# Performance work log

Hardware: AMD Instinct MI355X
Metric: run time of the kernel (lower is better)

## Reference

```python
import jax, jax.numpy as jnp
import numpy as np

TOKEN_SIZE = 16
STRIDE = 8
EMBED_DIM = 512


def setup_inputs() -> dict:
    key = jax.random.key(0)
    k1, k2 = jax.random.split(key)
    B, S, D = 32, 4096, EMBED_DIM
    x = jax.random.normal(k1, (B, S, D), dtype=jnp.float32)
    fan_in = TOKEN_SIZE * D
    W = jax.random.normal(k2, (fan_in, D), dtype=jnp.float32) / np.sqrt(fan_in)
    b = jnp.zeros((D,), dtype=jnp.float32)
    gamma = jnp.ones((D,), dtype=jnp.float32)
    beta = jnp.zeros((D,), dtype=jnp.float32)
    return {"x": x, "W": W, "b": b, "gamma": gamma, "beta": beta}


def reference(x, W, b, gamma, beta):
    B, S, D = x.shape
    n_win = (S - TOKEN_SIZE) // STRIDE + 1
    # gather all sliding windows at once: [n_win, token_size] index matrix
    idx = jnp.arange(n_win)[:, None] * STRIDE + jnp.arange(TOKEN_SIZE)[None, :]
    win = x[:, idx, :]                       # [B, n_win, token_size, D]
    win = win.reshape(B, n_win, TOKEN_SIZE * D)  # flatten each window
    h = jnp.einsum('bnf,fd->bnd', win, W) + b    # batched GEMM
    h = jax.nn.gelu(h, approximate=False)        # torch GELU default = exact erf
    # LayerNorm over last dim (eps matches torch default 1e-5)
    mu = jnp.mean(h, axis=-1, keepdims=True)
    var = jnp.var(h, axis=-1, keepdims=True)
    h = (h - mu) * jax.lax.rsqrt(var + 1e-5)
    return h * gamma + beta                      # [B, n_win, D]
```

## Files before the change

### kernel.cpp

```cpp
#include <hip/hip_runtime.h>
#include <hip/hip_bf16.h>
#include <cstdint>

#define S_LEN 4096
#define D_DIM 512
#define NWIN  511
#define KDIM  8192
#define THREADS 512

typedef __attribute__((ext_vector_type(8))) short short8;
typedef __attribute__((ext_vector_type(4))) float f32x4;

__device__ __forceinline__ unsigned short f2b(float f) {
    union { float f; unsigned int u; } v; v.f = f;
    unsigned int r = v.u + 0x7FFFu + ((v.u >> 16) & 1u);
    return (unsigned short)(r >> 16);
}

__global__ void wpack_kernel(const float* __restrict__ W, short8* __restrict__ pk) {
    __shared__ float tile[64][68];
    const int b2 = blockIdx.x;
    const int s = b2 >> 3, w = b2 & 7;
    const int t = s >> 3, c0 = (s & 7) << 6;
    const int tid = threadIdx.x;
    {
        int r = tid >> 2, c4 = (tid & 3) << 4;
        const float* src = W + (size_t)(t * 512 + c0 + r) * D_DIM + (w << 6) + c4;
#pragma unroll
        for (int j = 0; j < 4; ++j) {
            float4 v = *(const float4*)(src + 4 * j);
            tile[r][c4 + 4 * j + 0] = v.x;
            tile[r][c4 + 4 * j + 1] = v.y;
            tile[r][c4 + 4 * j + 2] = v.z;
            tile[r][c4 + 4 * j + 3] = v.w;
        }
    }
    __syncthreads();
    const int lane = tid & 63, f2 = tid >> 6;
#pragma unroll
    for (int ff = 0; ff < 2; ++ff) {
        int f = f2 * 2 + ff;
        int n = f >> 1, k32 = f & 1;
        short8 u;
#pragma unroll
        for (int e = 0; e < 8; ++e)
            u[e] = (short)f2b(tile[k32 * 32 + (lane >> 4) * 8 + e][n * 16 + (lane & 15)]);
        pk[((size_t)b2 * 8 + f) * 64 + lane] = u;
    }
}

__device__ __forceinline__ void load_b(const short8* __restrict__ pk, int s, int wid,
                                       int lane, short8 (&b)[4][2]) {
    const short8* base = pk + ((size_t)(s * 8 + wid) * 8) * 64 + lane;
#pragma unroll
    for (int n = 0; n < 4; ++n)
#pragma unroll
        for (int k32 = 0; k32 < 2; ++k32)
            b[n][k32] = base[(n * 2 + k32) * 64];
}

__global__ __launch_bounds__(THREADS, 2)
void fused_kernel(const float* __restrict__ x,
                  const short8* __restrict__ pk,
                  const float* __restrict__ bias,
                  const float* __restrict__ gamma,
                  const float* __restrict__ beta,
                  float* __restrict__ out)
{
    __shared__ __align__(16) unsigned short lsA[2][64 * 64];
    __shared__ float redS[8][64];
    __shared__ float redQ[8][64];

    const int blk = blockIdx.x;
    const int b  = blk >> 3;
    const int n0 = (blk & 7) << 6;
    const int tid = threadIdx.x;
    const int lane = tid & 63;
    const int wid  = tid >> 6;
    const int r15 = lane & 15, hi = lane >> 4;
    const int ai = tid >> 3, ak8 = tid & 7;
    const int akb = ak8 ^ (ai & 7);
    const float* xb = x + (size_t)b * S_LEN * D_DIM;

    f32x4 acc[4][4] = {};
    short8 bc[4][2], bn[4][2];

    {
        int row = 8 * (n0 + ai) + 0;
        if (row > S_LEN - 1) row = S_LEN - 1;
        const float* src = xb + (size_t)row * D_DIM + 0 + ak8 * 8;
        float4 f0 = *(const float4*)src;
        float4 f1 = *(const float4*)(src + 4);
        short8 u;
        u[0] = (short)f2b(f0.x); u[1] = (short)f2b(f0.y);
        u[2] = (short)f2b(f0.z); u[3] = (short)f2b(f0.w);
        u[4] = (short)f2b(f1.x); u[5] = (short)f2b(f1.y);
        u[6] = (short)f2b(f1.z); u[7] = (short)f2b(f1.w);
        *(short8*)&lsA[0][ai * 64 + akb * 8] = u;
        load_b(pk, 0, wid, lane, bc);
    }
    __syncthreads();

#define STEP(S, CUR, NXT, BCUR, BNXT)                                          \
    {                                                                          \
        const int sn = ((S) + 1) & 127;                                        \
                                            \
        const int tn = sn >> 3, c0n = (sn & 7) << 6;                           \
        int rown = 8 * (n0 + ai) + tn;                                         \
        if (rown > S_LEN - 1) rown = S_LEN - 1;                                \
        const float* asrc = xb + (size_t)rown * D_DIM + c0n + ak8 * 8;         \
        float4 f0 = *(const float4*)asrc;                                      \
        float4 f1 = *(const float4*)(asrc + 4);                                \
                                   \
        load_b(pk, sn, wid, lane, BNXT);                                       \
                                               \
        short8 afr[4][2];                                                      \
        _Pragma("unroll")                                                      \
        for (int m = 0; m < 4; ++m) {                                          \
            int row = 16 * m + r15;                                            \
            _Pragma("unroll")                                                  \
            for (int k32 = 0; k32 < 2; ++k32) {                                \
                int kb = (k32 * 4 + hi) ^ (row & 7);                           \
                afr[m][k32] = *(const short8*)&lsA[CUR][row * 64 + kb * 8];    \
            }                                                                  \
        }                                                                      \
               \
        _Pragma("unroll")                                                      \
        for (int k32 = 0; k32 < 2; ++k32)                                      \
            _Pragma("unroll")                                                  \
            for (int m = 0; m < 4; ++m)                                        \
                _Pragma("unroll")                                              \
                for (int n = 0; n < 4; ++n)                                    \
                    acc[m][n] = __builtin_amdgcn_mfma_f32_16x16x32_bf16(       \
                        afr[m][k32], BCUR[n][k32], acc[m][n], 0, 0, 0);        \
           \
        short8 u;                                                              \
        u[0] = (short)f2b(f0.x); u[1] = (short)f2b(f0.y);                      \
        u[2] = (short)f2b(f0.z); u[3] = (short)f2b(f0.w);                      \
        u[4] = (short)f2b(f1.x); u[5] = (short)f2b(f1.y);                      \
        u[6] = (short)f2b(f1.z); u[7] = (short)f2b(f1.w);                      \
        *(short8*)&lsA[NXT][ai * 64 + akb * 8] = u;                            \
        asm volatile("s_waitcnt lgkmcnt(0)" ::: "memory");                     \
        __builtin_amdgcn_s_barrier();                                          \
        __builtin_amdgcn_sched_barrier(0);                                     \
    }

    for (int it = 0; it < 64; ++it) {
        STEP(it * 2,     0, 1, bc, bn)
        STEP(it * 2 + 1, 1, 0, bn, bc)
    }
#undef STEP

    float bias4[4], gam4[4], bet4[4];
#pragma unroll
    for (int n = 0; n < 4; ++n) {
        int d = (wid << 6) + 16 * n + r15;
        bias4[n] = bias[d]; gam4[n] = gamma[d]; bet4[n] = beta[d];
    }
    float sum_[4][4], sq_[4][4];
#pragma unroll
    for (int m = 0; m < 4; ++m)
#pragma unroll
        for (int r = 0; r < 4; ++r) { sum_[m][r] = 0.f; sq_[m][r] = 0.f; }
#pragma unroll
    for (int m = 0; m < 4; ++m)
#pragma unroll
        for (int n = 0; n < 4; ++n)
#pragma unroll
            for (int r = 0; r < 4; ++r) {
                float h = acc[m][n][r] + bias4[n];
                float g = 0.5f * h * (1.0f + erff(h * 0.70710678118654752f));
                acc[m][n][r] = g;
                sum_[m][r] += g;
                sq_[m][r]  += g * g;
            }
#pragma unroll
    for (int m = 0; m < 4; ++m)
#pragma unroll
        for (int r = 0; r < 4; ++r) {
            float sv = sum_[m][r], qv = sq_[m][r];
#pragma unroll
            for (int msk = 1; msk < 16; msk <<= 1) {
                sv += __shfl_xor(sv, msk, 64);
                qv += __shfl_xor(qv, msk, 64);
            }
            sum_[m][r] = sv; sq_[m][r] = qv;
        }
    if (r15 == 0) {
#pragma unroll
        for (int m = 0; m < 4; ++m)
#pragma unroll
            for (int r = 0; r < 4; ++r) {
                int row16 = 16 * m + hi * 4 + r;
                redS[wid][row16] = sum_[m][r];
                redQ[wid][row16] = sq_[m][r];
            }
    }
    __syncthreads();
#pragma unroll
    for (int m = 0; m < 4; ++m) {
#pragma unroll
        for (int r = 0; r < 4; ++r) {
            int row16 = 16 * m + hi * 4 + r;
            float sv = 0.f, qv = 0.f;
#pragma unroll
            for (int w = 0; w < 8; ++w) { sv += redS[w][row16]; qv += redQ[w][row16]; }
            float mu  = sv * (1.0f / 512.0f);
            float var = qv * (1.0f / 512.0f) - mu * mu;
            float inv = rsqrtf(var + 1e-5f);
            int win = n0 + row16;
            if (win < NWIN) {
                size_t obase = ((size_t)b * NWIN + win) * D_DIM;
#pragma unroll
                for (int n = 0; n < 4; ++n) {
                    int d = (wid << 6) + 16 * n + r15;
                    out[obase + d] = (acc[m][n][r] - mu) * inv * gam4[n] + bet4[n];
                }
            }
        }
    }
}

__global__ void naive_kernel(const float* __restrict__ x, const float* __restrict__ W,
                             const float* __restrict__ bias, const float* __restrict__ gamma,
                             const float* __restrict__ beta, float* __restrict__ out) {
    __shared__ float hrow[D_DIM];
    __shared__ float red[2];
    const int b = blockIdx.x / NWIN, win = blockIdx.x % NWIN;
    const int d = threadIdx.x;
    float a = 0.f;
    for (int t = 0; t < 16; ++t) {
        const float* xr = x + ((size_t)b * S_LEN + 8 * win + t) * D_DIM;
        const float* wr = W + (size_t)t * D_DIM * D_DIM;
        for (int k = 0; k < D_DIM; ++k) a += xr[k] * wr[(size_t)k * D_DIM + d];
    }
    a += bias[d];
    a = 0.5f * a * (1.0f + erff(a * 0.70710678118654752f));
    hrow[d] = a;
    __syncthreads();
    if (d == 0) {
        float s = 0.f, q = 0.f;
        for (int k = 0; k < D_DIM; ++k) { s += hrow[k]; q += hrow[k] * hrow[k]; }
        float mu = s / D_DIM;
        red[0] = mu; red[1] = rsqrtf(q / D_DIM - mu * mu + 1e-5f);
    }
    __syncthreads();
    out[((size_t)b * NWIN + win) * D_DIM + d] = (a - red[0]) * red[1] * gamma[d] + beta[d];
}

extern "C" void kernel_launch(void* const* d_in, const int* in_sizes, int n_in,
                              void* d_out, int out_size, void* d_ws, size_t ws_size,
                              hipStream_t stream) {
    const float* x     = (const float*)d_in[0];
    const float* W     = (const float*)d_in[1];
    const float* bias  = (const float*)d_in[2];
    const float* gamma = (const float*)d_in[3];
    const float* beta  = (const float*)d_in[4];
    float* out = (float*)d_out;

    const size_t pk_bytes = (size_t)KDIM * D_DIM * sizeof(unsigned short);
    if (ws_size >= pk_bytes) {
        short8* pk = (short8*)d_ws;
        wpack_kernel<<<1024, 256, 0, stream>>>(W, (short8*)pk);
        fused_kernel<<<256, THREADS, 0, stream>>>(x, pk, bias, gamma, beta, out);
    } else {
        naive_kernel<<<32 * NWIN, D_DIM, 0, stream>>>(x, W, bias, gamma, beta, out);
    }
}
```

Baseline: 196.0 us.

## Split fused kernel into reuse-staged GEMM+GELU and separate LayerNorm kernel

Replaces the single fused kernel with a GEMM kernel that stages a contiguous 520-row slab of x per column chunk into LDS, so the overlapping sliding windows share the loaded rows instead of each token offset being re-read from global memory. Each block now covers half the output columns with 256 threads, giving 512 blocks. The GELU output goes to a workspace buffer, and a separate wave-per-row LayerNorm kernel then normalises it. This cuts redundant x loads and bf16 conversions, at the cost of writing and re-reading an intermediate h tensor, one extra launch, and barriers between the staging phases. It also depends on a larger workspace being available.

```diff
diff --git a/kernel.cpp b/kernel.cpp
--- a/kernel.cpp
+++ b/kernel.cpp
@@ -6,7 +6,8 @@
 #define D_DIM 512
 #define NWIN  511
 #define KDIM  8192
-#define THREADS 512
+#define TROWS 520
+#define ASLOTS (TROWS * 8)
 
 typedef __attribute__((ext_vector_type(8))) short short8;
 typedef __attribute__((ext_vector_type(4))) float f32x4;
@@ -49,9 +50,9 @@
     }
 }
 
-__device__ __forceinline__ void load_b(const short8* __restrict__ pk, int s, int wid,
+__device__ __forceinline__ void load_b(const short8* __restrict__ pk, int s, int wslot,
                                        int lane, short8 (&b)[4][2]) {
-    const short8* base = pk + ((size_t)(s * 8 + wid) * 8) * 64 + lane;
+    const short8* base = pk + ((size_t)(s * 8 + wslot) * 8) * 64 + lane;
 #pragma unroll
     for (int n = 0; n < 4; ++n)
 #pragma unroll
@@ -59,7 +60,165 @@
             b[n][k32] = base[(n * 2 + k32) * 64];
 }
 
-__global__ __launch_bounds__(THREADS, 2)
+__device__ __forceinline__ void stage_a(const float* __restrict__ xb, int n0, int tid,
+                                        int c0, unsigned short* __restrict__ lsA) {
+#pragma unroll 4
+    for (int it = 0; it < 17; ++it) {
+        int slot = tid + (it << 8);
+        if (slot < ASLOTS) {
+            int r = slot >> 3, k8 = slot & 7;
+            int grow = 8 * n0 + r;
+            if (grow > S_LEN - 1) grow = S_LEN - 1;
+            const float* src = xb + (size_t)grow * D_DIM + (c0 << 6) + (k8 << 3);
+            float4 a0 = *(const float4*)src;
+            float4 a1 = *(const float4*)(src + 4);
+            short8 u;
+            u[0] = (short)f2b(a0.x); u[1] = (short)f2b(a0.y);
+            u[2] = (short)f2b(a0.z); u[3] = (short)f2b(a0.w);
+            u[4] = (short)f2b(a1.x); u[5] = (short)f2b(a1.y);
+            u[6] = (short)f2b(a1.z); u[7] = (short)f2b(a1.w);
+            *(short8*)&lsA[(r << 6) + ((k8 ^ ((r >> 3) & 7)) << 3)] = u;
+        }
+    }
+}
+
+__global__ __launch_bounds__(256, 2)
+void gemm_kernel(const float* __restrict__ x,
+                 const short8* __restrict__ pk,
+                 const float* __restrict__ bias,
+                 float* __restrict__ hout)
+{
+    __shared__ __align__(16) unsigned short lsA[TROWS * 64];
+
+    const int p  = blockIdx.x;
+    const int g  = ((p >> 4) << 3) | (p & 7);
+    const int nc = (p >> 3) & 1;
+    const int b  = g >> 3;
+    const int n0 = (g & 7) << 6;
+    const int tid  = threadIdx.x;
+    const int lane = tid & 63, wid = tid >> 6;
+    const int wslot = nc * 4 + wid;
+    const int r15 = lane & 15, hi = lane >> 4;
+    const float* xb = x + (size_t)b * S_LEN * D_DIM;
+
+    f32x4 acc[4][4] = {};
+    short8 bc[4][2], bn[4][2];
+
+    load_b(pk, 0, wslot, lane, bc);
+    stage_a(xb, n0, tid, 0, lsA);
+    asm volatile("s_waitcnt lgkmcnt(0)" ::: "memory");
+    __builtin_amdgcn_s_barrier();
+    __builtin_amdgcn_sched_barrier(0);
+
+#define TSTEP(T, BCUR, BNXT)                                                   \
+    {                                                                          \
+        const int sn = ((T) < 15) ? (((T) + 1) * 8 + c0) : ((c0 + 1) & 7);     \
+        load_b(pk, sn, wslot, lane, BNXT);                                     \
+        short8 afr[4][2];                                                      \
+        _Pragma("unroll")                                                      \
+        for (int m = 0; m < 4; ++m) {                                          \
+            int row = (((m << 4) + r15) << 3) + (T);                           \
+            int sb  = (r15 + ((T) >> 3)) & 7;                                  \
+            _Pragma("unroll")                                                  \
+            for (int k32 = 0; k32 < 2; ++k32) {                                \
+                int swz = ((k32 << 2) + hi) ^ sb;                              \
+                afr[m][k32] = *(const short8*)&lsA[(row << 6) + (swz << 3)];   \
+            }                                                                  \
+        }                                                                      \
+        _Pragma("unroll")                                                      \
+        for (int k32 = 0; k32 < 2; ++k32)                                      \
+            _Pragma("unroll")                                                  \
+            for (int m = 0; m < 4; ++m)                                        \
+                _Pragma("unroll")                                              \
+                for (int n = 0; n < 4; ++n)                                    \
+                    acc[m][n] = __builtin_amdgcn_mfma_f32_16x16x32_bf16(       \
+                        afr[m][k32], BCUR[n][k32], acc[m][n], 0, 0, 0);        \
+    }
+
+    for (int c0 = 0; c0 < 8; ++c0) {
+#pragma unroll
+        for (int tt = 0; tt < 8; ++tt) {
+            TSTEP(2 * tt,     bc, bn)
+            TSTEP(2 * tt + 1, bn, bc)
+        }
+        __builtin_amdgcn_s_barrier();
+        __builtin_amdgcn_sched_barrier(0);
+        if (c0 < 7) {
+            stage_a(xb, n0, tid, c0 + 1, lsA);
+            asm volatile("s_waitcnt lgkmcnt(0)" ::: "memory");
+            __builtin_amdgcn_s_barrier();
+            __builtin_amdgcn_sched_barrier(0);
+        }
+    }
+#undef TSTEP
+
+    float bias4[4];
+#pragma unroll
+    for (int n = 0; n < 4; ++n)
+        bias4[n] = bias[(wslot << 6) + (n << 4) + r15];
+    float* hb = hout + (size_t)b * NWIN * D_DIM;
+#pragma unroll
+    for (int m = 0; m < 4; ++m) {
+#pragma unroll
+        for (int r = 0; r < 4; ++r) {
+            int win = n0 + (m << 4) + (hi << 2) + r;
+            if (win < NWIN) {
+                size_t obase = (size_t)win * D_DIM + (wslot << 6) + r15;
+#pragma unroll
+                for (int n = 0; n < 4; ++n) {
+                    float h = acc[m][n][r] + bias4[n];
+                    float gl = 0.5f * h * (1.0f + erff(h * 0.70710678118654752f));
+                    hb[obase + (n << 4)] = gl;
+                }
+            }
+        }
+    }
+}
+
+__global__ __launch_bounds__(256, 8)
+void ln_kernel(const float* __restrict__ h, const float* __restrict__ gamma,
+               const float* __restrict__ beta, float* __restrict__ out, int nrows)
+{
+    const int lane = threadIdx.x & 63;
+    const int wv = blockIdx.x * 4 + (threadIdx.x >> 6);
+    const int nw = gridDim.x * 4;
+    float gm[8], bt[8];
+#pragma unroll
+    for (int j = 0; j < 8; ++j) {
+        gm[j] = gamma[lane * 8 + j];
+        bt[j] = beta[lane * 8 + j];
+    }
+    for (int row = wv; row < nrows; row += nw) {
+        const float* src = h + (size_t)row * D_DIM + lane * 8;
+        float4 v0 = *(const float4*)src;
+        float4 v1 = *(const float4*)(src + 4);
+        float s = v0.x + v0.y + v0.z + v0.w + v1.x + v1.y + v1.z + v1.w;
+        float q = v0.x * v0.x + v0.y * v0.y + v0.z * v0.z + v0.w * v0.w +
+                  v1.x * v1.x + v1.y * v1.y + v1.z * v1.z + v1.w * v1.w;
+#pragma unroll
+        for (int msk = 1; msk < 64; msk <<= 1) {
+            s += __shfl_xor(s, msk, 64);
+            q += __shfl_xor(q, msk, 64);
+        }
+        float mu  = s * (1.0f / 512.0f);
+        float inv = rsqrtf(q * (1.0f / 512.0f) - mu * mu + 1e-5f);
+        float o[8] = { v0.x, v0.y, v0.z, v0.w, v1.x, v1.y, v1.z, v1.w };
+        float4 r0, r1;
+        r0.x = (o[0] - mu) * inv * gm[0] + bt[0];
+        r0.y = (o[1] - mu) * inv * gm[1] + bt[1];
+        r0.z = (o[2] - mu) * inv * gm[2] + bt[2];
+        r0.w = (o[3] - mu) * inv * gm[3] + bt[3];
+        r1.x = (o[4] - mu) * inv * gm[4] + bt[4];
+        r1.y = (o[5] - mu) * inv * gm[5] + bt[5];
+        r1.z = (o[6] - mu) * inv * gm[6] + bt[6];
+        r1.w = (o[7] - mu) * inv * gm[7] + bt[7];
+        float* dst = out + (size_t)row * D_DIM + lane * 8;
+        *(float4*)dst = r0;
+        *(float4*)(dst + 4) = r1;
+    }
+}
+
+__global__ __launch_bounds__(512, 2)
 void fused_kernel(const float* __restrict__ x,
                   const short8* __restrict__ pk,
                   const float* __restrict__ bias,
@@ -84,7 +243,6 @@
 
     f32x4 acc[4][4] = {};
     short8 bc[4][2], bn[4][2];
-
     {
         int row = 8 * (n0 + ai) + 0;
         if (row > S_LEN - 1) row = S_LEN - 1;
@@ -104,16 +262,13 @@
 #define STEP(S, CUR, NXT, BCUR, BNXT)                                          \
     {                                                                          \
         const int sn = ((S) + 1) & 127;                                        \
-                                            \
         const int tn = sn >> 3, c0n = (sn & 7) << 6;                           \
         int rown = 8 * (n0 + ai) + tn;                                         \
         if (rown > S_LEN - 1) rown = S_LEN - 1;                                \
         const float* asrc = xb + (size_t)rown * D_DIM + c0n + ak8 * 8;         \
         float4 f0 = *(const float4*)asrc;                                      \
         float4 f1 = *(const float4*)(asrc + 4);                                \
-                                   \
         load_b(pk, sn, wid, lane, BNXT);                                       \
-                                               \
         short8 afr[4][2];                                                      \
         _Pragma("unroll")                                                      \
         for (int m = 0; m < 4; ++m) {                                          \
@@ -124,7 +279,6 @@
                 afr[m][k32] = *(const short8*)&lsA[CUR][row * 64 + kb * 8];    \
             }                                                                  \
         }                                                                      \
-               \
         _Pragma("unroll")                                                      \
         for (int k32 = 0; k32 < 2; ++k32)                                      \
             _Pragma("unroll")                                                  \
@@ -133,7 +287,6 @@
                 for (int n = 0; n < 4; ++n)                                    \
                     acc[m][n] = __builtin_amdgcn_mfma_f32_16x16x32_bf16(       \
                         afr[m][k32], BCUR[n][k32], acc[m][n], 0, 0, 0);        \
-           \
         short8 u;                                                              \
         u[0] = (short)f2b(f0.x); u[1] = (short)f2b(f0.y);                      \
         u[2] = (short)f2b(f0.z); u[3] = (short)f2b(f0.w);                      \
@@ -259,10 +412,18 @@
     float* out = (float*)d_out;
 
     const size_t pk_bytes = (size_t)KDIM * D_DIM * sizeof(unsigned short);
-    if (ws_size >= pk_bytes) {
+    const size_t h_bytes  = (size_t)32 * NWIN * D_DIM * sizeof(float);
+
+    if (ws_size >= pk_bytes + h_bytes) {
         short8* pk = (short8*)d_ws;
-        wpack_kernel<<<1024, 256, 0, stream>>>(W, (short8*)pk);
-        fused_kernel<<<256, THREADS, 0, stream>>>(x, pk, bias, gamma, beta, out);
+        float* hbuf = (float*)((char*)d_ws + pk_bytes);
+        wpack_kernel<<<1024, 256, 0, stream>>>(W, pk);
+        gemm_kernel<<<512, 256, 0, stream>>>(x, pk, bias, hbuf);
+        ln_kernel<<<1024, 256, 0, stream>>>(hbuf, gamma, beta, out, 32 * NWIN);
+    } else if (ws_size >= pk_bytes) {
+        short8* pk = (short8*)d_ws;
+        wpack_kernel<<<1024, 256, 0, stream>>>(W, pk);
+        fused_kernel<<<256, 512, 0, stream>>>(x, pk, bias, gamma, beta, out);
     } else {
         naive_kernel<<<32 * NWIN, D_DIM, 0, stream>>>(x, W, bias, gamma, beta, out);
     }
```

Result: slower. 208.2 us (+6.2%).
